# Kernel optimization log

Measured on AMD Instinct MI355X. Metric: run time of the kernel, lower is better.

The kernel has to match this reference:

```python
import jax, jax.numpy as jnp
import numpy as np

H, DK, DV, D = 16, 64, 64, 1024  # num_heads, q/k size, v size, embedding_dim


def setup_inputs() -> dict:
    key = jax.random.key(0)
    k1, k2, k3, k4 = jax.random.split(key, 4)
    scale = 1.0 / np.sqrt(D)
    X = jax.random.normal(k1, (4, 2048, D), dtype=jnp.float32)
    # stacked per-head projection weights (one Linear per head in the original ModuleList)
    Wq = jax.random.normal(k2, (H, D, DK), dtype=jnp.float32) * scale
    Wk = jax.random.normal(k3, (H, D, DK), dtype=jnp.float32) * scale
    Wv = jax.random.normal(k4, (H, D, DV), dtype=jnp.float32) * scale
    return {"X": X, "Wq": Wq, "Wk": Wk, "Wv": Wv}


def reference(X, Wq, Wk, Wv):
    # Batched equivalent of looping over per-head attention layers and concatenating.
    q = jnp.einsum("bsd,hde->bhse", X, Wq)  # [B,H,S,DK]
    k = jnp.einsum("bsd,hde->bhse", X, Wk)  # [B,H,S,DK]
    v = jnp.einsum("bsd,hde->bhse", X, Wv)  # [B,H,S,DV]
    scores = jnp.einsum("bhqe,bhke->bhqk", q, k) / jnp.sqrt(jnp.asarray(DK, q.dtype))
    attn = jax.nn.softmax(scores, axis=-1)
    out = jnp.einsum("bhqk,bhke->bhqe", attn, v)  # [B,H,S,DV]
    B, _, S, _ = out.shape
    # concat over heads along last dim (head order preserved)
    return out.transpose(0, 2, 1, 3).reshape(B, S, H * DV)
```

## Files before the change

### kernel.cpp

```cpp
#include <hip/hip_runtime.h>
#include <hip/hip_bf16.h>
#include <stdint.h>

typedef __attribute__((ext_vector_type(8))) short bf16x8;
typedef __attribute__((ext_vector_type(4))) float f32x4;
typedef __attribute__((ext_vector_type(16))) float f32x16;

__device__ __forceinline__ unsigned short f2bf(float f) {
  union { float f; unsigned u; } v; v.f = f;
  unsigned r = (v.u + 0x7FFFu + ((v.u >> 16) & 1u)) >> 16;
  return (unsigned short)r;
}

__device__ __forceinline__ void gload16(const void* g, void* l) {
  __builtin_amdgcn_global_load_lds(
      (const __attribute__((address_space(1))) void*)g,
      (__attribute__((address_space(3))) void*)l, 16, 0, 0);
}

__device__ __forceinline__ bf16x8 lds_read8(const unsigned short* base, int row, int k0) {
  int byteoff = row * 128 + (((k0 >> 3) ^ (row & 7)) << 4);
  return *(const bf16x8*)((const char*)base + byteoff);
}

__device__ __forceinline__ bf16x8 lds_at(const unsigned short* smem, unsigned off) {
  return *(const bf16x8*)((const char*)smem + off);
}

__device__ __forceinline__ unsigned int cvtpk(float a, float b) {
  unsigned int r;
  asm("v_cvt_pk_bf16_f32 %0, %1, %2" : "=v"(r) : "v"(a), "v"(b));
  return r;
}

__global__ void cvt_x_kernel(const float* __restrict__ X, unsigned short* __restrict__ Xb) {
  int i = blockIdx.x * blockDim.x + threadIdx.x;
  const float4* src = (const float4*)X;
  float4 a = src[2 * i];
  float4 b = src[2 * i + 1];
  bf16x8 o;
  o[0] = (short)f2bf(a.x); o[1] = (short)f2bf(a.y);
  o[2] = (short)f2bf(a.z); o[3] = (short)f2bf(a.w);
  o[4] = (short)f2bf(b.x); o[5] = (short)f2bf(b.y);
  o[6] = (short)f2bf(b.z); o[7] = (short)f2bf(b.w);
  *(bf16x8*)(Xb + (size_t)i * 8) = o;
}

__global__ void cvt_w_kernel(const float* __restrict__ Wq, const float* __restrict__ Wk,
                             const float* __restrict__ Wv, unsigned short* __restrict__ Wbt) {
  __shared__ float t[64][65];
  const int k0 = blockIdx.x * 64;
  const int h  = blockIdx.y;
  const int p  = blockIdx.z;
  const float* W = (p == 0 ? Wq : (p == 1 ? Wk : Wv)) + (size_t)h * 1024 * 64;
  const int tid = threadIdx.x;
  {
    int e = tid & 63, kq = tid >> 6;
#pragma unroll
    for (int i = 0; i < 16; ++i) {
      int k = i * 4 + kq;
      t[k][e] = W[(size_t)(k0 + k) * 64 + e];
    }
  }
  __syncthreads();
  {
    int k = tid & 63, eq = tid >> 6;
#pragma unroll
    for (int i = 0; i < 16; ++i) {
      int e = i * 4 + eq;
      Wbt[(size_t)((p * 1024) + h * 64 + e) * 1024 + k0 + k] = f2bf(t[k][e]);
    }
  }
}

__global__ __launch_bounds__(256, 2) void proj_gemm(
    const unsigned short* __restrict__ Xb,
    const unsigned short* __restrict__ Wbt,
    unsigned short* __restrict__ Qb,
    unsigned short* __restrict__ Kb,
    unsigned short* __restrict__ Vt) {
  __shared__ unsigned short As[128 * 64];
  __shared__ unsigned short Bs[128 * 64];
  const int m0 = blockIdx.x * 128;
  const int n0 = blockIdx.y * 128;
  const int p  = blockIdx.z;
  const int tid = threadIdx.x;
  const int lane = tid & 63;
  const int wid = tid >> 6;
  const int wr = wid >> 1, wc = wid & 1;

  const unsigned short* Ag = Xb + (size_t)m0 * 1024;
  const unsigned short* Bg = Wbt + (size_t)p * 1024 * 1024 + (size_t)n0 * 1024;

  f32x4 acc[4][4];
#pragma unroll
  for (int i = 0; i < 4; ++i)
#pragma unroll
    for (int j = 0; j < 4; ++j) acc[i][j] = (f32x4){0.f, 0.f, 0.f, 0.f};

  for (int kt = 0; kt < 16; ++kt) {
#pragma unroll
    for (int i = 0; i < 4; ++i) {
      int row0 = wid * 32 + i * 8;
      int lr = row0 + (lane >> 3);
      int slot = (lane & 7) ^ (lr & 7);
      gload16(Ag + (size_t)lr * 1024 + kt * 64 + slot * 8, (char*)As + row0 * 128);
      gload16(Bg + (size_t)lr * 1024 + kt * 64 + slot * 8, (char*)Bs + row0 * 128);
    }
    __syncthreads();
#pragma unroll
    for (int ks = 0; ks < 2; ++ks) {
      int k0 = ks * 32 + (lane >> 4) * 8;
      bf16x8 a[4], b[4];
#pragma unroll
      for (int mi = 0; mi < 4; ++mi) a[mi] = lds_read8(As, wr * 64 + mi * 16 + (lane & 15), k0);
#pragma unroll
      for (int ni = 0; ni < 4; ++ni) b[ni] = lds_read8(Bs, wc * 64 + ni * 16 + (lane & 15), k0);
#pragma unroll
      for (int mi = 0; mi < 4; ++mi)
#pragma unroll
        for (int ni = 0; ni < 4; ++ni)
          acc[mi][ni] = __builtin_amdgcn_mfma_f32_16x16x32_bf16(a[mi], b[ni], acc[mi][ni], 0, 0, 0);
    }
    __syncthreads();
  }

#pragma unroll
  for (int mi = 0; mi < 4; ++mi) {
    int m = m0 + wr * 64 + mi * 16 + ((lane >> 4) << 2);
    int bb = m >> 11;
    int s  = m & 2047;
#pragma unroll
    for (int ni = 0; ni < 4; ++ni) {
      int n = n0 + wc * 64 + ni * 16 + (lane & 15);
      int h = n >> 6, e = n & 63;
#pragma unroll
      for (int r = 0; r < 4; ++r) {
        float v = acc[mi][ni][r];
        int sr = s + r;
        if (p == 0) {
          Qb[((size_t)(bb * 16 + h) * 2048 + sr) * 64 + e] = f2bf(v * 0.18033688f);
        } else if (p == 1) {
          Kb[((size_t)(bb * 16 + h) * 2048 + sr) * 64 + e] = f2bf(v);
        } else {
          int spos = (sr & ~12) | ((sr & 4) << 1) | ((sr & 8) >> 1);
          Vt[((size_t)(bb * 16 + h) * 64 + e) * 2048 + spos] = f2bf(v);
        }
      }
    }
  }
}

__global__ __launch_bounds__(256, 2) void attn_kernel(
    const unsigned short* __restrict__ Qb,
    const unsigned short* __restrict__ Kb,
    const unsigned short* __restrict__ Vt,
    float* __restrict__ out) {
  __shared__ unsigned short smem[16384];
  const int bh = blockIdx.x;
  const int q0 = blockIdx.y * 256;
  const int tid = threadIdx.x;
  const int lane = tid & 63;
  const int wid = tid >> 6;
  const int ql = lane & 31;
  const int hi = lane >> 5;

  const unsigned short* Qp = Qb + (size_t)bh * 2048 * 64;
  const unsigned short* Kp = Kb + (size_t)bh * 2048 * 64;
  const unsigned short* Vp = Vt + (size_t)bh * 64 * 2048;

  bf16x8 qf0[4], qf1[4];
#pragma unroll
  for (int ks = 0; ks < 4; ++ks) {
    qf0[ks] = *(const bf16x8*)(Qp + (size_t)(q0 + wid * 64 + ql) * 64 + ks * 16 + hi * 8);
    qf1[ks] = *(const bf16x8*)(Qp + (size_t)(q0 + wid * 64 + 32 + ql) * 64 + ks * 16 + hi * 8);
  }

  f32x16 a00, a01, a10, a11;
#pragma unroll
  for (int i = 0; i < 16; ++i) { a00[i] = 0.f; a01[i] = 0.f; a10[i] = 0.f; a11[i] = 0.f; }
  float l0 = 0.f, l1 = 0.f;

  const unsigned lane_off = (unsigned)(ql * 128 + (((ql & 7) ^ hi) << 4));

  auto STAGE = [&](int buf, int kt) {
    unsigned short* Ks = smem + buf * 8192;
    unsigned short* Vs = Ks + 4096;
#pragma unroll
    for (int i = 0; i < 2; ++i) {
      int row0 = wid * 16 + i * 8;
      int lr = row0 + (lane >> 3);
      int slot = (lane & 7) ^ (lr & 7);
      gload16(Kp + (size_t)(kt * 64 + lr) * 64 + slot * 8, (char*)Ks + row0 * 128);
      gload16(Vp + (size_t)lr * 2048 + kt * 64 + slot * 8, (char*)Vs + row0 * 128);
    }
  };

  STAGE(0, 0);
  asm volatile("s_waitcnt vmcnt(0)" ::: "memory");
  __builtin_amdgcn_s_barrier();

  int cur = 0;
  for (int kt = 0; kt < 32; ++kt) {
    if (kt < 31) STAGE(cur ^ 1, kt + 1);
    const unsigned cb = (unsigned)cur << 14;

#pragma unroll
    for (int t = 0; t < 2; ++t) {
      bf16x8 kf[4];
#pragma unroll
      for (int ks = 0; ks < 4; ++ks)
        kf[ks] = lds_at(smem, lane_off ^ (cb | (t << 12) | (ks << 5)));

      f32x16 s0, s1;
#pragma unroll
      for (int i = 0; i < 16; ++i) { s0[i] = 0.f; s1[i] = 0.f; }
#pragma unroll
      for (int ks = 0; ks < 4; ++ks) {
        s0 = __builtin_amdgcn_mfma_f32_32x32x16_bf16(kf[ks], qf0[ks], s0, 0, 0, 0);
        s1 = __builtin_amdgcn_mfma_f32_32x32x16_bf16(kf[ks], qf1[ks], s1, 0, 0, 0);
      }

#pragma unroll
      for (int i = 0; i < 16; ++i) { s0[i] = exp2f(s0[i]); s1[i] = exp2f(s1[i]); }

      {
        float sm0[8], sm1[8];
#pragma unroll
        for (int i = 0; i < 8; ++i) { sm0[i] = s0[i] + s0[i + 8]; sm1[i] = s1[i] + s1[i + 8]; }
        l0 += ((sm0[0] + sm0[1]) + (sm0[2] + sm0[3])) + ((sm0[4] + sm0[5]) + (sm0[6] + sm0[7]));
        l1 += ((sm1[0] + sm1[1]) + (sm1[2] + sm1[3])) + ((sm1[4] + sm1[5]) + (sm1[6] + sm1[7]));
      }

      union { unsigned int u[4]; bf16x8 v; } P00, P01, P10, P11;
#pragma unroll
      for (int j = 0; j < 4; ++j) {
        P00.u[j] = cvtpk(s0[2 * j],     s0[2 * j + 1]);
        P01.u[j] = cvtpk(s0[8 + 2 * j], s0[8 + 2 * j + 1]);
        P10.u[j] = cvtpk(s1[2 * j],     s1[2 * j + 1]);
        P11.u[j] = cvtpk(s1[8 + 2 * j], s1[8 + 2 * j + 1]);
      }

      bf16x8 vf00 = lds_at(smem, lane_off ^ (cb | 8192u | (0 << 12) | (t << 6) | (0 << 5)));
      bf16x8 vf01 = lds_at(smem, lane_off ^ (cb | 8192u | (0 << 12) | (t << 6) | (1 << 5)));
      bf16x8 vf10 = lds_at(smem, lane_off ^ (cb | 8192u | (1 << 12) | (t << 6) | (0 << 5)));
      bf16x8 vf11 = lds_at(smem, lane_off ^ (cb | 8192u | (1 << 12) | (t << 6) | (1 << 5)));

      a00 = __builtin_amdgcn_mfma_f32_32x32x16_bf16(vf00, P00.v, a00, 0, 0, 0);
      a10 = __builtin_amdgcn_mfma_f32_32x32x16_bf16(vf00, P10.v, a10, 0, 0, 0);
      a00 = __builtin_amdgcn_mfma_f32_32x32x16_bf16(vf01, P01.v, a00, 0, 0, 0);
      a10 = __builtin_amdgcn_mfma_f32_32x32x16_bf16(vf01, P11.v, a10, 0, 0, 0);
      a01 = __builtin_amdgcn_mfma_f32_32x32x16_bf16(vf10, P00.v, a01, 0, 0, 0);
      a11 = __builtin_amdgcn_mfma_f32_32x32x16_bf16(vf10, P10.v, a11, 0, 0, 0);
      a01 = __builtin_amdgcn_mfma_f32_32x32x16_bf16(vf11, P01.v, a01, 0, 0, 0);
      a11 = __builtin_amdgcn_mfma_f32_32x32x16_bf16(vf11, P11.v, a11, 0, 0, 0);
    }

    asm volatile("s_waitcnt vmcnt(0)" ::: "memory");
    __builtin_amdgcn_s_barrier();
    cur ^= 1;
  }

  __builtin_amdgcn_s_barrier();

  const int b = bh >> 4, h = bh & 15;
  float* fs = (float*)smem + wid * 2048;

#pragma unroll
  for (int g = 0; g < 2; ++g) {
    float lg = g ? l1 : l0;
    float lf = lg + __shfl_xor(lg, 32, 64);
    float inv = 1.0f / lf;
    const f32x16& m0v = g ? a10 : a00;
    const f32x16& m1v = g ? a11 : a01;
#pragma unroll
    for (int r = 0; r < 16; ++r) {
      int e0 = (r & 3) + 8 * (r >> 2) + 4 * hi;
      fs[ql * 64 + (e0 ^ ql)] = m0v[r] * inv;
      int e1 = 32 + e0;
      fs[ql * 64 + (e1 ^ ql)] = m1v[r] * inv;
    }
#pragma unroll
    for (int i = 0; i < 32; ++i) {
      float v = fs[i * 64 + (lane ^ i)];
      out[((size_t)(b * 2048 + q0 + wid * 64 + g * 32 + i)) * 1024 + h * 64 + lane] = v;
    }
  }
}

extern "C" void kernel_launch(void* const* d_in, const int* in_sizes, int n_in,
                              void* d_out, int out_size, void* d_ws, size_t ws_size,
                              hipStream_t stream) {
  (void)in_sizes; (void)n_in; (void)out_size; (void)ws_size;
  const float* X  = (const float*)d_in[0];
  const float* Wq = (const float*)d_in[1];
  const float* Wk = (const float*)d_in[2];
  const float* Wv = (const float*)d_in[3];
  float* out = (float*)d_out;

  unsigned short* Xb  = (unsigned short*)d_ws;
  unsigned short* Wbt = Xb + (size_t)8192 * 1024;
  unsigned short* Qb  = Wbt + (size_t)3 * 1024 * 1024;
  unsigned short* Kb  = Qb + (size_t)64 * 2048 * 64;
  unsigned short* Vt  = Kb + (size_t)64 * 2048 * 64;

  hipLaunchKernelGGL(cvt_x_kernel, dim3(4096), dim3(256), 0, stream, X, Xb);
  hipLaunchKernelGGL(cvt_w_kernel, dim3(16, 16, 3), dim3(256), 0, stream, Wq, Wk, Wv, Wbt);
  hipLaunchKernelGGL(proj_gemm, dim3(64, 8, 3), dim3(256), 0, stream, Xb, Wbt, Qb, Kb, Vt);
  hipLaunchKernelGGL(attn_kernel, dim3(64, 8), dim3(256), 0, stream, Qb, Kb, Vt, out);
}
```

Before: 171.8 us.

## Double KV tile to 128 keys per stage and use hardware exp2

Widens each staged K/V tile from 64 to 128 keys, which halves the number of outer loop iterations and the barriers/waits between stages. Shared memory doubles to 64 KB per block and the V layout becomes 256-byte rows with a matching swizzle. It also replaces exp2f with the raw v_exp_f32 instruction to drop the range-handling code around it. The cost is higher LDS use, which may limit occupancy under the two-blocks-per-CU launch bound.

```diff
diff --git a/kernel.cpp b/kernel.cpp
--- a/kernel.cpp
+++ b/kernel.cpp
@@ -10,6 +10,14 @@
   union { float f; unsigned u; } v; v.f = f;
   unsigned r = (v.u + 0x7FFFu + ((v.u >> 16) & 1u)) >> 16;
   return (unsigned short)r;
+}
+
+__device__ __forceinline__ float fexp2(float x) {
+#if __has_builtin(__builtin_amdgcn_exp2f)
+  return __builtin_amdgcn_exp2f(x);
+#else
+  float r; asm("v_exp_f32 %0, %1" : "=v"(r) : "v"(x)); return r;
+#endif
 }
 
 __device__ __forceinline__ void gload16(const void* g, void* l) {
@@ -156,7 +164,7 @@
     const unsigned short* __restrict__ Kb,
     const unsigned short* __restrict__ Vt,
     float* __restrict__ out) {
-  __shared__ unsigned short smem[16384];
+  __shared__ unsigned short smem[32768];
   const int bh = blockIdx.x;
   const int q0 = blockIdx.y * 256;
   const int tid = threadIdx.x;
@@ -181,18 +189,25 @@
   for (int i = 0; i < 16; ++i) { a00[i] = 0.f; a01[i] = 0.f; a10[i] = 0.f; a11[i] = 0.f; }
   float l0 = 0.f, l1 = 0.f;
 
-  const unsigned lane_off = (unsigned)(ql * 128 + (((ql & 7) ^ hi) << 4));
+  const unsigned lane_offK = (unsigned)(ql * 128 + (((ql & 7) ^ hi) << 4));
+  const unsigned lane_offV = (unsigned)(16384 + ql * 256 + (((ql & 7) ^ hi) << 4));
 
   auto STAGE = [&](int buf, int kt) {
-    unsigned short* Ks = smem + buf * 8192;
-    unsigned short* Vs = Ks + 4096;
-#pragma unroll
-    for (int i = 0; i < 2; ++i) {
-      int row0 = wid * 16 + i * 8;
-      int lr = row0 + (lane >> 3);
-      int slot = (lane & 7) ^ (lr & 7);
-      gload16(Kp + (size_t)(kt * 64 + lr) * 64 + slot * 8, (char*)Ks + row0 * 128);
-      gload16(Vp + (size_t)lr * 2048 + kt * 64 + slot * 8, (char*)Vs + row0 * 128);
+    unsigned short* Ks = smem + buf * 16384;
+    unsigned short* Vs = Ks + 8192;
+#pragma unroll
+    for (int i = 0; i < 4; ++i) {
+      int row0 = i * 32 + wid * 8;
+      int row = row0 + (lane >> 3);
+      int slot = (lane & 7) ^ (row & 7);
+      gload16(Kp + (size_t)(kt * 128 + row) * 64 + slot * 8, (char*)Ks + row0 * 128);
+    }
+#pragma unroll
+    for (int i = 0; i < 4; ++i) {
+      int row0 = i * 16 + wid * 4;
+      int row = row0 + (lane >> 4);
+      int slot = (lane & 15) ^ (row & 7);
+      gload16(Vp + (size_t)row * 2048 + kt * 128 + slot * 8, (char*)Vs + row0 * 256);
     }
   };
 
@@ -201,16 +216,16 @@
   __builtin_amdgcn_s_barrier();
 
   int cur = 0;
-  for (int kt = 0; kt < 32; ++kt) {
-    if (kt < 31) STAGE(cur ^ 1, kt + 1);
-    const unsigned cb = (unsigned)cur << 14;
-
-#pragma unroll
-    for (int t = 0; t < 2; ++t) {
+  for (int kt = 0; kt < 16; ++kt) {
+    if (kt < 15) STAGE(cur ^ 1, kt + 1);
+    const unsigned cb = (unsigned)cur << 15;
+
+#pragma unroll
+    for (int t = 0; t < 4; ++t) {
       bf16x8 kf[4];
 #pragma unroll
       for (int ks = 0; ks < 4; ++ks)
-        kf[ks] = lds_at(smem, lane_off ^ (cb | (t << 12) | (ks << 5)));
+        kf[ks] = lds_at(smem, lane_offK ^ (cb | (t << 12) | (ks << 5)));
 
       f32x16 s0, s1;
 #pragma unroll
@@ -222,7 +237,7 @@
       }
 
 #pragma unroll
-      for (int i = 0; i < 16; ++i) { s0[i] = exp2f(s0[i]); s1[i] = exp2f(s1[i]); }
+      for (int i = 0; i < 16; ++i) { s0[i] = fexp2(s0[i]); s1[i] = fexp2(s1[i]); }
 
       {
         float sm0[8], sm1[8];
@@ -241,10 +256,10 @@
         P11.u[j] = cvtpk(s1[8 + 2 * j], s1[8 + 2 * j + 1]);
       }
 
-      bf16x8 vf00 = lds_at(smem, lane_off ^ (cb | 8192u | (0 << 12) | (t << 6) | (0 << 5)));
-      bf16x8 vf01 = lds_at(smem, lane_off ^ (cb | 8192u | (0 << 12) | (t << 6) | (1 << 5)));
-      bf16x8 vf10 = lds_at(smem, lane_off ^ (cb | 8192u | (1 << 12) | (t << 6) | (0 << 5)));
-      bf16x8 vf11 = lds_at(smem, lane_off ^ (cb | 8192u | (1 << 12) | (t << 6) | (1 << 5)));
+      bf16x8 vf00 = lds_at(smem, lane_offV ^ (cb | (0 << 13) | (t << 6) | (0 << 5)));
+      bf16x8 vf01 = lds_at(smem, lane_offV ^ (cb | (0 << 13) | (t << 6) | (1 << 5)));
+      bf16x8 vf10 = lds_at(smem, lane_offV ^ (cb | (1 << 13) | (t << 6) | (0 << 5)));
+      bf16x8 vf11 = lds_at(smem, lane_offV ^ (cb | (1 << 13) | (t << 6) | (1 << 5)));
 
       a00 = __builtin_amdgcn_mfma_f32_32x32x16_bf16(vf00, P00.v, a00, 0, 0, 0);
       a10 = __builtin_amdgcn_mfma_f32_32x32x16_bf16(vf00, P10.v, a10, 0, 0, 0);
```

Measured after the change: 156.5 us. 1.1x faster.
